# Optimization experiments

Measured on AMD Instinct MI355X. Metric: run time of the kernel, lower is better.

## Reference

```python
import jax, jax.numpy as jnp
import numpy as np

DIM = 1024
NUM_HEADS = 16
HEAD_DIM = DIM // NUM_HEADS
SCALE = HEAD_DIM ** (-0.5)


def alibi_slopes(num_heads):
    x = (2 ** 8) ** (1.0 / num_heads)
    return jnp.array([1.0 / x ** (i + 1) for i in range(num_heads)], dtype=jnp.float32)


def setup_inputs() -> dict:
    key = jax.random.key(0)
    ks = jax.random.split(key, 6)
    B, N = 2, 2048
    x = jax.random.normal(ks[0], (B, N, DIM), dtype=jnp.float32)
    s = DIM ** -0.5
    Wq = jax.random.normal(ks[1], (DIM, DIM), dtype=jnp.float32) * s
    Wk = jax.random.normal(ks[2], (DIM, DIM), dtype=jnp.float32) * s
    Wv = jax.random.normal(ks[3], (DIM, DIM), dtype=jnp.float32) * s
    Wp = jax.random.normal(ks[4], (DIM, DIM), dtype=jnp.float32) * s
    bp = jnp.zeros((DIM,), dtype=jnp.float32)
    return {"x": x, "Wq": Wq, "Wk": Wk, "Wv": Wv, "Wp": Wp, "bp": bp}


def reference(x, Wq, Wk, Wv, Wp, bp):
    B, N, C = x.shape
    H, D = NUM_HEADS, HEAD_DIM
    # Linear layers use torch convention: y = x @ W.T
    q = (x @ Wq.T).reshape(B, N, H, D).transpose(0, 2, 1, 3)  # [B,H,N,D]
    k = (x @ Wk.T).reshape(B, N, H, D).transpose(0, 2, 1, 3)
    v = (x @ Wv.T).reshape(B, N, H, D).transpose(0, 2, 1, 3)
    # ALiBi bias: slopes[h] * (j - i), shape [H,N,N]
    rel = (jnp.arange(N)[None, :] - jnp.arange(N)[:, None]).astype(jnp.float32)
    bias = alibi_slopes(H)[:, None, None] * rel  # [H,N,N]
    # NOTE: original code DIVIDES by scale (= head_dim**-0.5), i.e. multiplies by sqrt(D)
    score = jnp.einsum("bhnd,bhmd->bhnm", q, k) / SCALE + bias[None]
    attn = jax.nn.softmax(score, axis=-1)
    out = jnp.einsum("bhnm,bhmd->bhnd", attn, v)
    out = out.transpose(0, 2, 1, 3).reshape(B, N, C)
    return out @ Wp.T + bp
```

## Files before the change

### kernel.cpp

```cpp
#include <hip/hip_runtime.h>
#include <hip/hip_bf16.h>
#include <cstdint>
#include <cstddef>

#define BB 2
#define NN 2048
#define CC 1024
#define HH 16
#define DD 64
#define MM (BB*NN)

typedef __attribute__((ext_vector_type(8))) _Float16 half8;
typedef __attribute__((ext_vector_type(4))) _Float16 half4;
typedef __attribute__((ext_vector_type(4))) float f32x4;

__device__ __forceinline__ float exp2_fast(float x) {
    float r; asm("v_exp_f32 %0, %1" : "=v"(r) : "v"(x)); return r;
}

__device__ __forceinline__ void gl_lds16(const void* g, void* l) {
    __builtin_amdgcn_global_load_lds(
        (const __attribute__((address_space(1))) unsigned int*)g,
        (__attribute__((address_space(3))) unsigned int*)l, 16, 0, 0);
}

__global__ __launch_bounds__(256) void cvt16(
    const float* __restrict__ in, _Float16* __restrict__ out, int n4) {
    int i = blockIdx.x * 256 + threadIdx.x;
    if (i >= n4) return;
    float4 v = ((const float4*)in)[i];
    half4 h = { (_Float16)v.x, (_Float16)v.y, (_Float16)v.z, (_Float16)v.w };
    ((half4*)out)[i] = h;
}

__global__ __launch_bounds__(256) void cvt16w(
    const float* __restrict__ w0, const float* __restrict__ w1,
    const float* __restrict__ w2, const float* __restrict__ w3,
    _Float16* __restrict__ out, int n4) {
    int s = blockIdx.y;
    const float* in = (s == 0) ? w0 : (s == 1) ? w1 : (s == 2) ? w2 : w3;
    _Float16* dst = out + (size_t)s * n4 * 4;
    int i = blockIdx.x * 256 + threadIdx.x;
    if (i >= n4) return;
    float4 v = ((const float4*)in)[i];
    half4 h = { (_Float16)v.x, (_Float16)v.y, (_Float16)v.z, (_Float16)v.w };
    ((half4*)dst)[i] = h;
}

template<int MODE, bool HASBIAS>
__global__ __launch_bounds__(256) void gemm16(
    const _Float16* __restrict__ A, const _Float16* __restrict__ B,
    const float* __restrict__ bias, float* __restrict__ Cout,
    _Float16* __restrict__ Oh, float scale, int M, int N, int K) {
    __shared__ _Float16 sA[64 * 64];
    __shared__ _Float16 sB[64 * 64];

    const int t = threadIdx.x;
    const int bm = blockIdx.y, bn = blockIdx.x;
    const int w = t >> 6, lane = t & 63;
    const int wr = (w >> 1) * 32, wc = (w & 1) * 32;
    const int lr = lane & 15, lg = lane >> 4;

    f32x4 acc[2][2];
#pragma unroll
    for (int a = 0; a < 2; ++a)
#pragma unroll
        for (int b2 = 0; b2 < 2; ++b2)
#pragma unroll
            for (int e = 0; e < 4; ++e) acc[a][b2][e] = 0.f;

    for (int kt = 0; kt < K; kt += 64) {
#pragma unroll
        for (int p = 0; p < 2; ++p) {
            int u = p * 256 + t;
            int rowu = u >> 3, su = (u & 7) ^ (rowu & 7);
            gl_lds16(A + (size_t)(bm * 64 + rowu) * K + kt + su * 8, sA + u * 8);
            gl_lds16(B + (size_t)(bn * 64 + rowu) * K + kt + su * 8, sB + u * 8);
        }
        __syncthreads();

#pragma unroll
        for (int c = 0; c < 2; ++c) {
            half8 a0, a1, b0, b1;
            {
                int r0 = wr + lr, r1 = wr + 16 + lr;
                a0 = *(const half8*)((const char*)sA + ((r0 * 128 + c * 64 + lg * 16) ^ ((r0 & 7) << 4)));
                a1 = *(const half8*)((const char*)sA + ((r1 * 128 + c * 64 + lg * 16) ^ ((r1 & 7) << 4)));
                int q0 = wc + lr, q1 = wc + 16 + lr;
                b0 = *(const half8*)((const char*)sB + ((q0 * 128 + c * 64 + lg * 16) ^ ((q0 & 7) << 4)));
                b1 = *(const half8*)((const char*)sB + ((q1 * 128 + c * 64 + lg * 16) ^ ((q1 & 7) << 4)));
            }
            acc[0][0] = __builtin_amdgcn_mfma_f32_16x16x32_f16(a0, b0, acc[0][0], 0, 0, 0);
            acc[0][1] = __builtin_amdgcn_mfma_f32_16x16x32_f16(a0, b1, acc[0][1], 0, 0, 0);
            acc[1][0] = __builtin_amdgcn_mfma_f32_16x16x32_f16(a1, b0, acc[1][0], 0, 0, 0);
            acc[1][1] = __builtin_amdgcn_mfma_f32_16x16x32_f16(a1, b1, acc[1][1], 0, 0, 0);
        }
        __syncthreads();
    }

#pragma unroll
    for (int fi = 0; fi < 2; ++fi)
#pragma unroll
        for (int fj = 0; fj < 2; ++fj)
#pragma unroll
            for (int e = 0; e < 4; ++e) {
                int row = bm * 64 + wr + fi * 16 + lg * 4 + e;
                int col = bn * 64 + wc + fj * 16 + lr;
                float v = acc[fi][fj][e];
                if (MODE == 0) {
                    if (HASBIAS) v += bias[col];
                    Cout[(size_t)row * N + col] = v;
                } else {
                    int b2 = row >> 11, n2 = row & (NN - 1);
                    int h2 = col >> 6, d2 = col & (DD - 1);
                    if (MODE == 2) {
                        Oh[((size_t)(b2 * HH + h2) * NN + n2) * DD + d2] = (_Float16)(v * scale);
                    } else {
                        Oh[((size_t)(b2 * HH + h2) * DD + d2) * NN + n2] = (_Float16)v;
                    }
                }
            }
}

__global__ __launch_bounds__(256) void attn16(
    const _Float16* __restrict__ Qh, const _Float16* __restrict__ Kh,
    const _Float16* __restrict__ Vt, _Float16* __restrict__ AO) {
    __shared__ _Float16 sK[2][64 * 64];
    __shared__ _Float16 sV[2][64 * 64];
    __shared__ _Float16 sP[4][16 * 64];

    const int t = threadIdx.x, w = t >> 6, lane = t & 63;
    const int lr = lane & 15, lg = lane >> 4;
    const int qb = blockIdx.x, bh = blockIdx.y;
    const int b = bh >> 4, h = bh & 15;
    const int i0 = qb * 64;
    const size_t baseND = (size_t)bh * NN * DD;
    const size_t baseDN = (size_t)bh * DD * NN;

    half8 qf[2];
    {
        const size_t qoff = baseND + (size_t)(i0 + w * 16 + lr) * DD;
        qf[0] = *(const half8*)(Qh + qoff + 0 * 32 + lg * 8);
        qf[1] = *(const half8*)(Qh + qoff + 1 * 32 + lg * 8);
    }

    f32x4 accO[4];
#pragma unroll
    for (int e = 0; e < 4; ++e)
        accO[e][0] = accO[e][1] = accO[e][2] = accO[e][3] = 0.f;
    float m_run = -INFINITY, l_run = 0.f;

    const float slope2 = exp2f(-0.5f * (float)(h + 1)) * 1.44269504f;
    f32x4 cini[4];
#pragma unroll
    for (int ct = 0; ct < 4; ++ct)
#pragma unroll
        for (int e = 0; e < 4; ++e)
            cini[ct][e] = slope2 * (float)(ct * 16 + lg * 4 + e);

    auto stage = [&](int buf, int jt) {
#pragma unroll
        for (int p = 0; p < 2; ++p) {
            int u = p * 256 + t;
            int rowu = u >> 3, su = (u & 7) ^ (rowu & 7);
            gl_lds16(Kh + baseND + (size_t)(jt * 64 + rowu) * DD + su * 8, &sK[buf][u * 8]);
            gl_lds16(Vt + baseDN + (size_t)rowu * NN + jt * 64 + su * 8, &sV[buf][u * 8]);
        }
    };

    stage(0, 0);
    __syncthreads();
    int cur = 0;
    float tb = 0.f;

    for (int jt = 0; jt < NN / 64; ++jt) {
        if (jt + 1 < NN / 64) stage(cur ^ 1, jt + 1);

        f32x4 s[4];
#pragma unroll
        for (int ct = 0; ct < 4; ++ct)
#pragma unroll
            for (int e = 0; e < 4; ++e) s[ct][e] = tb + cini[ct][e];

        __builtin_amdgcn_s_setprio(1);
#pragma unroll
        for (int ct = 0; ct < 4; ++ct) {
#pragma unroll
            for (int c = 0; c < 2; ++c) {
                int row = ct * 16 + lr;
                half8 kf = *(const half8*)((const char*)&sK[cur][0] +
                    ((row * 128 + c * 64 + lg * 16) ^ ((row & 7) << 4)));
                s[ct] = __builtin_amdgcn_mfma_f32_16x16x32_f16(kf, qf[c], s[ct], 0, 0, 0);
            }
        }
        __builtin_amdgcn_s_setprio(0);

        float x0 = fmaxf(fmaxf(s[0][0], s[0][1]), fmaxf(s[0][2], s[0][3]));
        float x1 = fmaxf(fmaxf(s[1][0], s[1][1]), fmaxf(s[1][2], s[1][3]));
        float x2 = fmaxf(fmaxf(s[2][0], s[2][1]), fmaxf(s[2][2], s[2][3]));
        float x3 = fmaxf(fmaxf(s[3][0], s[3][1]), fmaxf(s[3][2], s[3][3]));
        float mx = fmaxf(fmaxf(x0, x1), fmaxf(x2, x3));
        mx = fmaxf(mx, __shfl_xor(mx, 16, 64));
        mx = fmaxf(mx, __shfl_xor(mx, 32, 64));
        float mnew = fmaxf(m_run, mx);
        float al = exp2_fast(m_run - mnew);
#pragma unroll
        for (int ct = 0; ct < 4; ++ct)
#pragma unroll
            for (int e = 0; e < 4; ++e) s[ct][e] = exp2_fast(s[ct][e] - mnew);
        float y0 = (s[0][0] + s[0][1]) + (s[0][2] + s[0][3]);
        float y1 = (s[1][0] + s[1][1]) + (s[1][2] + s[1][3]);
        float y2 = (s[2][0] + s[2][1]) + (s[2][2] + s[2][3]);
        float y3 = (s[3][0] + s[3][1]) + (s[3][2] + s[3][3]);
        float sum = (y0 + y1) + (y2 + y3);
        sum += __shfl_xor(sum, 16, 64);
        sum += __shfl_xor(sum, 32, 64);
        m_run = mnew;
        l_run = l_run * al + sum;

#pragma unroll
        for (int ct = 0; ct < 4; ++ct) {
            half4 pk = { (_Float16)s[ct][0], (_Float16)s[ct][1],
                         (_Float16)s[ct][2], (_Float16)s[ct][3] };
            *(half4*)((char*)sP[w] + ((lr * 128 + ct * 32 + lg * 8) ^ ((lr & 7) << 4))) = pk;
        }

#pragma unroll
        for (int ctd = 0; ctd < 4; ++ctd)
#pragma unroll
            for (int e = 0; e < 4; ++e) accO[ctd][e] *= al;

        half8 pb0 = *(const half8*)((const char*)sP[w] + ((lr * 128 + 0 * 64 + lg * 16) ^ ((lr & 7) << 4)));
        half8 pb1 = *(const half8*)((const char*)sP[w] + ((lr * 128 + 1 * 64 + lg * 16) ^ ((lr & 7) << 4)));
        __builtin_amdgcn_s_setprio(1);
#pragma unroll
        for (int ctd = 0; ctd < 4; ++ctd) {
#pragma unroll
            for (int c = 0; c < 2; ++c) {
                int row = ctd * 16 + lr;
                half8 vf = *(const half8*)((const char*)&sV[cur][0] +
                    ((row * 128 + c * 64 + lg * 16) ^ ((row & 7) << 4)));
                accO[ctd] = __builtin_amdgcn_mfma_f32_16x16x32_f16(vf, c ? pb1 : pb0, accO[ctd], 0, 0, 0);
            }
        }
        __builtin_amdgcn_s_setprio(0);

        __syncthreads();
        cur ^= 1;
        tb += slope2 * 64.f;
    }

    float rl = 1.0f / l_run;
    const size_t obase = ((size_t)b * NN + i0 + w * 16 + lr) * CC + h * DD;
#pragma unroll
    for (int ctd = 0; ctd < 4; ++ctd) {
        half4 ov = { (_Float16)(accO[ctd][0] * rl), (_Float16)(accO[ctd][1] * rl),
                     (_Float16)(accO[ctd][2] * rl), (_Float16)(accO[ctd][3] * rl) };
        *(half4*)(AO + obase + ctd * 16 + lg * 4) = ov;
    }
}

extern "C" void kernel_launch(void* const* d_in, const int* in_sizes, int n_in,
                              void* d_out, int out_size, void* d_ws, size_t ws_size,
                              hipStream_t stream) {
    const float* x  = (const float*)d_in[0];
    const float* Wq = (const float*)d_in[1];
    const float* Wk = (const float*)d_in[2];
    const float* Wv = (const float*)d_in[3];
    const float* Wp = (const float*)d_in[4];
    const float* bp = (const float*)d_in[5];
    float* out = (float*)d_out;

    char* ws = (char*)d_ws;
    const size_t MB = 1024 * 1024;
    _Float16* X16 = (_Float16*)(ws + 0 * MB);
    _Float16* W16 = (_Float16*)(ws + 8 * MB);
    _Float16* QH  = (_Float16*)(ws + 16 * MB);
    _Float16* KH  = (_Float16*)(ws + 24 * MB);
    _Float16* VT  = (_Float16*)(ws + 32 * MB);
    _Float16* AO  = (_Float16*)(ws + 40 * MB);
    _Float16* WQ16 = W16;
    _Float16* WK16 = W16 + 1024 * 1024;
    _Float16* WV16 = W16 + 2 * 1024 * 1024;
    _Float16* WP16 = W16 + 3 * 1024 * 1024;

    cvt16<<<4096, 256, 0, stream>>>(x, X16, (MM * CC) / 4);
    cvt16w<<<dim3(1024, 4), 256, 0, stream>>>(Wq, Wk, Wv, Wp, W16, (CC * CC) / 4);

    dim3 gg(CC / 64, MM / 64);
    const float QSCALE = 8.0f * 1.44269504f;
    gemm16<2, false><<<gg, 256, 0, stream>>>(X16, WQ16, nullptr, nullptr, QH, QSCALE, MM, CC, CC);
    gemm16<2, false><<<gg, 256, 0, stream>>>(X16, WK16, nullptr, nullptr, KH, 1.0f,   MM, CC, CC);
    gemm16<3, false><<<gg, 256, 0, stream>>>(X16, WV16, nullptr, nullptr, VT, 1.0f,   MM, CC, CC);

    attn16<<<dim3(NN / 64, BB * HH), 256, 0, stream>>>(QH, KH, VT, AO);

    gemm16<0, true><<<gg, 256, 0, stream>>>(AO, WP16, bp, out, nullptr, 1.0f, MM, CC, CC);
}
```

Before: 158.2 us.

## Fuse QKV GEMMs into one 128x128-tile kernel and double attention query rows

The three Q/K/V projections become a single GEMM over the concatenated weights, using 128x128 tiles with a 4x4 MFMA fragment per wave, and V is written to its transposed layout with packed half4 stores. The attention kernel now gives each wave 32 query rows, so every K/V fragment loaded from shared memory feeds two MFMAs. It also adds a lazy-rescale rule that skips the max update and the accumulator rescale when the new max exceeds the running max by at most 8 (in log2 units). These changes cut launch count and shared-memory traffic per FLOP, at the cost of more registers, lower occupancy and half as many attention blocks.

```diff
diff --git a/kernel.cpp b/kernel.cpp
--- a/kernel.cpp
+++ b/kernel.cpp
@@ -47,11 +47,87 @@
     ((half4*)dst)[i] = h;
 }
 
-template<int MODE, bool HASBIAS>
-__global__ __launch_bounds__(256) void gemm16(
+__global__ __launch_bounds__(256) void gemmQKV(
     const _Float16* __restrict__ A, const _Float16* __restrict__ B,
-    const float* __restrict__ bias, float* __restrict__ Cout,
-    _Float16* __restrict__ Oh, float scale, int M, int N, int K) {
+    _Float16* __restrict__ QH, _Float16* __restrict__ KH,
+    _Float16* __restrict__ VT, float qscale) {
+    __shared__ _Float16 sA[128 * 64];
+    __shared__ _Float16 sB[128 * 64];
+    const int K = CC;
+
+    const int t = threadIdx.x;
+    const int bm = blockIdx.y, bn = blockIdx.x;
+    const int w = t >> 6, lane = t & 63;
+    const int wr = (w >> 1) * 64, wc = (w & 1) * 64;
+    const int lr = lane & 15, lg = lane >> 4;
+
+    f32x4 acc[4][4];
+#pragma unroll
+    for (int a = 0; a < 4; ++a)
+#pragma unroll
+        for (int b2 = 0; b2 < 4; ++b2)
+#pragma unroll
+            for (int e = 0; e < 4; ++e) acc[a][b2][e] = 0.f;
+
+    for (int kt = 0; kt < K; kt += 64) {
+#pragma unroll
+        for (int p = 0; p < 4; ++p) {
+            int u = p * 256 + t;
+            int rowu = u >> 3, su = (u & 7) ^ (rowu & 7);
+            gl_lds16(A + (size_t)(bm * 128 + rowu) * K + kt + su * 8, sA + u * 8);
+            gl_lds16(B + (size_t)(bn * 128 + rowu) * K + kt + su * 8, sB + u * 8);
+        }
+        __syncthreads();
+
+#pragma unroll
+        for (int c = 0; c < 2; ++c) {
+            half8 af[4], bf[4];
+#pragma unroll
+            for (int f = 0; f < 4; ++f) {
+                int ra = wr + f * 16 + lr;
+                af[f] = *(const half8*)((const char*)sA + ((ra * 128 + c * 64 + lg * 16) ^ ((ra & 7) << 4)));
+                int rb = wc + f * 16 + lr;
+                bf[f] = *(const half8*)((const char*)sB + ((rb * 128 + c * 64 + lg * 16) ^ ((rb & 7) << 4)));
+            }
+#pragma unroll
+            for (int fi = 0; fi < 4; ++fi)
+#pragma unroll
+                for (int fj = 0; fj < 4; ++fj)
+                    acc[fi][fj] = __builtin_amdgcn_mfma_f32_16x16x32_f16(af[fi], bf[fj], acc[fi][fj], 0, 0, 0);
+        }
+        __syncthreads();
+    }
+
+#pragma unroll
+    for (int fi = 0; fi < 4; ++fi)
+#pragma unroll
+        for (int fj = 0; fj < 4; ++fj) {
+            int col = bn * 128 + wc + fj * 16 + lr;
+            int sel = col >> 10, c10 = col & 1023;
+            int h2 = c10 >> 6, d2 = c10 & 63;
+            int rowb = bm * 128 + wr + fi * 16 + lg * 4;
+            int b2 = rowb >> 11, n2 = rowb & (NN - 1);
+            if (sel == 0) {
+#pragma unroll
+                for (int e = 0; e < 4; ++e)
+                    QH[((size_t)(b2 * HH + h2) * NN + n2 + e) * DD + d2] =
+                        (_Float16)(acc[fi][fj][e] * qscale);
+            } else if (sel == 1) {
+#pragma unroll
+                for (int e = 0; e < 4; ++e)
+                    KH[((size_t)(b2 * HH + h2) * NN + n2 + e) * DD + d2] =
+                        (_Float16)acc[fi][fj][e];
+            } else {
+                half4 pk = { (_Float16)acc[fi][fj][0], (_Float16)acc[fi][fj][1],
+                             (_Float16)acc[fi][fj][2], (_Float16)acc[fi][fj][3] };
+                *(half4*)(VT + ((size_t)(b2 * HH + h2) * DD + d2) * NN + n2) = pk;
+            }
+        }
+}
+
+__global__ __launch_bounds__(256) void gemmPROJ(
+    const _Float16* __restrict__ A, const _Float16* __restrict__ B,
+    const float* __restrict__ bias, float* __restrict__ Cout, int M, int N, int K) {
     __shared__ _Float16 sA[64 * 64];
     __shared__ _Float16 sB[64 * 64];
 
@@ -106,19 +182,7 @@
             for (int e = 0; e < 4; ++e) {
                 int row = bm * 64 + wr + fi * 16 + lg * 4 + e;
                 int col = bn * 64 + wc + fj * 16 + lr;
-                float v = acc[fi][fj][e];
-                if (MODE == 0) {
-                    if (HASBIAS) v += bias[col];
-                    Cout[(size_t)row * N + col] = v;
-                } else {
-                    int b2 = row >> 11, n2 = row & (NN - 1);
-                    int h2 = col >> 6, d2 = col & (DD - 1);
-                    if (MODE == 2) {
-                        Oh[((size_t)(b2 * HH + h2) * NN + n2) * DD + d2] = (_Float16)(v * scale);
-                    } else {
-                        Oh[((size_t)(b2 * HH + h2) * DD + d2) * NN + n2] = (_Float16)v;
-                    }
-                }
+                Cout[(size_t)row * N + col] = acc[fi][fj][e] + bias[col];
             }
 }
 
@@ -127,30 +191,36 @@
     const _Float16* __restrict__ Vt, _Float16* __restrict__ AO) {
     __shared__ _Float16 sK[2][64 * 64];
     __shared__ _Float16 sV[2][64 * 64];
-    __shared__ _Float16 sP[4][16 * 64];
+    __shared__ _Float16 sP[4][32 * 64];
 
     const int t = threadIdx.x, w = t >> 6, lane = t & 63;
     const int lr = lane & 15, lg = lane >> 4;
     const int qb = blockIdx.x, bh = blockIdx.y;
     const int b = bh >> 4, h = bh & 15;
-    const int i0 = qb * 64;
+    const int i0 = qb * 128;
     const size_t baseND = (size_t)bh * NN * DD;
     const size_t baseDN = (size_t)bh * DD * NN;
 
-    half8 qf[2];
-    {
-        const size_t qoff = baseND + (size_t)(i0 + w * 16 + lr) * DD;
-        qf[0] = *(const half8*)(Qh + qoff + 0 * 32 + lg * 8);
-        qf[1] = *(const half8*)(Qh + qoff + 1 * 32 + lg * 8);
-    }
-
-    f32x4 accO[4];
-#pragma unroll
-    for (int e = 0; e < 4; ++e)
-        accO[e][0] = accO[e][1] = accO[e][2] = accO[e][3] = 0.f;
-    float m_run = -INFINITY, l_run = 0.f;
+    half8 qf[2][2];
+#pragma unroll
+    for (int u = 0; u < 2; ++u) {
+        const size_t qoff = baseND + (size_t)(i0 + w * 32 + u * 16 + lr) * DD;
+        qf[u][0] = *(const half8*)(Qh + qoff + 0 * 32 + lg * 8);
+        qf[u][1] = *(const half8*)(Qh + qoff + 1 * 32 + lg * 8);
+    }
+
+    f32x4 accO[2][4];
+    float m_run[2], l_run[2];
+#pragma unroll
+    for (int u = 0; u < 2; ++u) {
+        m_run[u] = -INFINITY; l_run[u] = 0.f;
+#pragma unroll
+        for (int c2 = 0; c2 < 4; ++c2)
+            accO[u][c2][0] = accO[u][c2][1] = accO[u][c2][2] = accO[u][c2][3] = 0.f;
+    }
 
     const float slope2 = exp2f(-0.5f * (float)(h + 1)) * 1.44269504f;
+    const float s64 = slope2 * 64.f;
     f32x4 cini[4];
 #pragma unroll
     for (int ct = 0; ct < 4; ++ct)
@@ -176,87 +246,109 @@
     for (int jt = 0; jt < NN / 64; ++jt) {
         if (jt + 1 < NN / 64) stage(cur ^ 1, jt + 1);
 
-        f32x4 s[4];
+        f32x4 s[2][4];
+#pragma unroll
+        for (int u = 0; u < 2; ++u)
+#pragma unroll
+            for (int ct = 0; ct < 4; ++ct) s[u][ct] = cini[ct];
+
+        __builtin_amdgcn_s_setprio(1);
 #pragma unroll
         for (int ct = 0; ct < 4; ++ct)
-#pragma unroll
-            for (int e = 0; e < 4; ++e) s[ct][e] = tb + cini[ct][e];
-
-        __builtin_amdgcn_s_setprio(1);
-#pragma unroll
-        for (int ct = 0; ct < 4; ++ct) {
 #pragma unroll
             for (int c = 0; c < 2; ++c) {
                 int row = ct * 16 + lr;
                 half8 kf = *(const half8*)((const char*)&sK[cur][0] +
                     ((row * 128 + c * 64 + lg * 16) ^ ((row & 7) << 4)));
-                s[ct] = __builtin_amdgcn_mfma_f32_16x16x32_f16(kf, qf[c], s[ct], 0, 0, 0);
-            }
-        }
+                s[0][ct] = __builtin_amdgcn_mfma_f32_16x16x32_f16(kf, qf[0][c], s[0][ct], 0, 0, 0);
+                s[1][ct] = __builtin_amdgcn_mfma_f32_16x16x32_f16(kf, qf[1][c], s[1][ct], 0, 0, 0);
+            }
         __builtin_amdgcn_s_setprio(0);
 
-        float x0 = fmaxf(fmaxf(s[0][0], s[0][1]), fmaxf(s[0][2], s[0][3]));
-        float x1 = fmaxf(fmaxf(s[1][0], s[1][1]), fmaxf(s[1][2], s[1][3]));
-        float x2 = fmaxf(fmaxf(s[2][0], s[2][1]), fmaxf(s[2][2], s[2][3]));
-        float x3 = fmaxf(fmaxf(s[3][0], s[3][1]), fmaxf(s[3][2], s[3][3]));
-        float mx = fmaxf(fmaxf(x0, x1), fmaxf(x2, x3));
-        mx = fmaxf(mx, __shfl_xor(mx, 16, 64));
-        mx = fmaxf(mx, __shfl_xor(mx, 32, 64));
-        float mnew = fmaxf(m_run, mx);
-        float al = exp2_fast(m_run - mnew);
-#pragma unroll
-        for (int ct = 0; ct < 4; ++ct)
-#pragma unroll
-            for (int e = 0; e < 4; ++e) s[ct][e] = exp2_fast(s[ct][e] - mnew);
-        float y0 = (s[0][0] + s[0][1]) + (s[0][2] + s[0][3]);
-        float y1 = (s[1][0] + s[1][1]) + (s[1][2] + s[1][3]);
-        float y2 = (s[2][0] + s[2][1]) + (s[2][2] + s[2][3]);
-        float y3 = (s[3][0] + s[3][1]) + (s[3][2] + s[3][3]);
-        float sum = (y0 + y1) + (y2 + y3);
-        sum += __shfl_xor(sum, 16, 64);
-        sum += __shfl_xor(sum, 32, 64);
-        m_run = mnew;
-        l_run = l_run * al + sum;
-
-#pragma unroll
-        for (int ct = 0; ct < 4; ++ct) {
-            half4 pk = { (_Float16)s[ct][0], (_Float16)s[ct][1],
-                         (_Float16)s[ct][2], (_Float16)s[ct][3] };
-            *(half4*)((char*)sP[w] + ((lr * 128 + ct * 32 + lg * 8) ^ ((lr & 7) << 4))) = pk;
-        }
-
+#pragma unroll
+        for (int u = 0; u < 2; ++u) {
+            float x0 = fmaxf(fmaxf(s[u][0][0], s[u][0][1]), fmaxf(s[u][0][2], s[u][0][3]));
+            float x1 = fmaxf(fmaxf(s[u][1][0], s[u][1][1]), fmaxf(s[u][1][2], s[u][1][3]));
+            float x2 = fmaxf(fmaxf(s[u][2][0], s[u][2][1]), fmaxf(s[u][2][2], s[u][2][3]));
+            float x3 = fmaxf(fmaxf(s[u][3][0], s[u][3][1]), fmaxf(s[u][3][2], s[u][3][3]));
+            float mx = fmaxf(fmaxf(x0, x1), fmaxf(x2, x3));
+            mx = fmaxf(mx, __shfl_xor(mx, 16, 64));
+            mx = fmaxf(mx, __shfl_xor(mx, 32, 64));
+            float mxt = mx + tb;
+            float msh;
+            bool defer = __all(mxt <= m_run[u] + 8.f) != 0;
+            if (defer) {
+                msh = m_run[u] - tb;
+            } else {
+                float mnew = fmaxf(m_run[u], mxt);
+                float al = exp2_fast(m_run[u] - mnew);
+                m_run[u] = mnew;
+                msh = mnew - tb;
+#pragma unroll
+                for (int c2 = 0; c2 < 4; ++c2)
+#pragma unroll
+                    for (int e = 0; e < 4; ++e) accO[u][c2][e] *= al;
+                l_run[u] *= al;
+            }
+#pragma unroll
+            for (int ct = 0; ct < 4; ++ct)
+#pragma unroll
+                for (int e = 0; e < 4; ++e) s[u][ct][e] = exp2_fast(s[u][ct][e] - msh);
+            float y0 = (s[u][0][0] + s[u][0][1]) + (s[u][0][2] + s[u][0][3]);
+            float y1 = (s[u][1][0] + s[u][1][1]) + (s[u][1][2] + s[u][1][3]);
+            float y2 = (s[u][2][0] + s[u][2][1]) + (s[u][2][2] + s[u][2][3]);
+            float y3 = (s[u][3][0] + s[u][3][1]) + (s[u][3][2] + s[u][3][3]);
+            float sum = (y0 + y1) + (y2 + y3);
+            sum += __shfl_xor(sum, 16, 64);
+            sum += __shfl_xor(sum, 32, 64);
+            l_run[u] += sum;
+
+#pragma unroll
+            for (int ct = 0; ct < 4; ++ct) {
+                half4 pk = { (_Float16)s[u][ct][0], (_Float16)s[u][ct][1],
+                             (_Float16)s[u][ct][2], (_Float16)s[u][ct][3] };
+                int row = u * 16 + lr;
+                *(half4*)((char*)sP[w] + ((row * 128 + ct * 32 + lg * 8) ^ ((lr & 7) << 4))) = pk;
+            }
+        }
+
+        half8 pb[2][2];
+#pragma unroll
+        for (int u = 0; u < 2; ++u)
+#pragma unroll
+            for (int c = 0; c < 2; ++c) {
+                int row = u * 16 + lr;
+                pb[u][c] = *(const half8*)((const char*)sP[w] +
+                    ((row * 128 + c * 64 + lg * 16) ^ ((lr & 7) << 4)));
+            }
+        __builtin_amdgcn_s_setprio(1);
 #pragma unroll
         for (int ctd = 0; ctd < 4; ++ctd)
-#pragma unroll
-            for (int e = 0; e < 4; ++e) accO[ctd][e] *= al;
-
-        half8 pb0 = *(const half8*)((const char*)sP[w] + ((lr * 128 + 0 * 64 + lg * 16) ^ ((lr & 7) << 4)));
-        half8 pb1 = *(const half8*)((const char*)sP[w] + ((lr * 128 + 1 * 64 + lg * 16) ^ ((lr & 7) << 4)));
-        __builtin_amdgcn_s_setprio(1);
-#pragma unroll
-        for (int ctd = 0; ctd < 4; ++ctd) {
 #pragma unroll
             for (int c = 0; c < 2; ++c) {
                 int row = ctd * 16 + lr;
                 half8 vf = *(const half8*)((const char*)&sV[cur][0] +
                     ((row * 128 + c * 64 + lg * 16) ^ ((row & 7) << 4)));
-                accO[ctd] = __builtin_amdgcn_mfma_f32_16x16x32_f16(vf, c ? pb1 : pb0, accO[ctd], 0, 0, 0);
-            }
-        }
+                accO[0][ctd] = __builtin_amdgcn_mfma_f32_16x16x32_f16(vf, pb[0][c], accO[0][ctd], 0, 0, 0);
+                accO[1][ctd] = __builtin_amdgcn_mfma_f32_16x16x32_f16(vf, pb[1][c], accO[1][ctd], 0, 0, 0);
+            }
         __builtin_amdgcn_s_setprio(0);
 
         __syncthreads();
         cur ^= 1;
-        tb += slope2 * 64.f;
-    }
-
-    float rl = 1.0f / l_run;
-    const size_t obase = ((size_t)b * NN + i0 + w * 16 + lr) * CC + h * DD;
-#pragma unroll
-    for (int ctd = 0; ctd < 4; ++ctd) {
-        half4 ov = { (_Float16)(accO[ctd][0] * rl), (_Float16)(accO[ctd][1] * rl),
-                     (_Float16)(accO[ctd][2] * rl), (_Float16)(accO[ctd][3] * rl) };
-        *(half4*)(AO + obase + ctd * 16 + lg * 4) = ov;
+        tb += s64;
+    }
+
+#pragma unroll
+    for (int u = 0; u < 2; ++u) {
+        float rl = 1.0f / l_run[u];
+        const size_t obase = ((size_t)b * NN + i0 + w * 32 + u * 16 + lr) * CC + h * DD;
+#pragma unroll
+        for (int ctd = 0; ctd < 4; ++ctd) {
+            half4 ov = { (_Float16)(accO[u][ctd][0] * rl), (_Float16)(accO[u][ctd][1] * rl),
+                         (_Float16)(accO[u][ctd][2] * rl), (_Float16)(accO[u][ctd][3] * rl) };
+            *(half4*)(AO + obase + ctd * 16 + lg * 4) = ov;
+        }
     }
 }
 
@@ -279,21 +371,15 @@
     _Float16* KH  = (_Float16*)(ws + 24 * MB);
     _Float16* VT  = (_Float16*)(ws + 32 * MB);
     _Float16* AO  = (_Float16*)(ws + 40 * MB);
-    _Float16* WQ16 = W16;
-    _Float16* WK16 = W16 + 1024 * 1024;
-    _Float16* WV16 = W16 + 2 * 1024 * 1024;
     _Float16* WP16 = W16 + 3 * 1024 * 1024;
 
     cvt16<<<4096, 256, 0, stream>>>(x, X16, (MM * CC) / 4);
     cvt16w<<<dim3(1024, 4), 256, 0, stream>>>(Wq, Wk, Wv, Wp, W16, (CC * CC) / 4);
 
-    dim3 gg(CC / 64, MM / 64);
     const float QSCALE = 8.0f * 1.44269504f;
-    gemm16<2, false><<<gg, 256, 0, stream>>>(X16, WQ16, nullptr, nullptr, QH, QSCALE, MM, CC, CC);
-    gemm16<2, false><<<gg, 256, 0, stream>>>(X16, WK16, nullptr, nullptr, KH, 1.0f,   MM, CC, CC);
-    gemm16<3, false><<<gg, 256, 0, stream>>>(X16, WV16, nullptr, nullptr, VT, 1.0f,   MM, CC, CC);
-
-    attn16<<<dim3(NN / 64, BB * HH), 256, 0, stream>>>(QH, KH, VT, AO);
-
-    gemm16<0, true><<<gg, 256, 0, stream>>>(AO, WP16, bp, out, nullptr, 1.0f, MM, CC, CC);
-}
+    gemmQKV<<<dim3(3 * CC / 128, MM / 128), 256, 0, stream>>>(X16, W16, QH, KH, VT, QSCALE);
+
+    attn16<<<dim3(NN / 128, BB * HH), 256, 0, stream>>>(QH, KH, VT, AO);
+
+    gemmPROJ<<<dim3(CC / 64, MM / 64), 256, 0, stream>>>(AO, WP16, bp, out, MM, CC, CC);
+}
```

Result: faster. 152.8 us (-3.4%).
